# Optimization experiments

Hardware: AMD Instinct MI355X
Metric: run time of the kernel (lower is better)

The kernel has to match this reference:

```python
import jax, jax.numpy as jnp
import numpy as np

B, C, L = 128, 12, 1024
N_DIL, DIV, H, K, KSZ, NCP = 7, 2, 32, 8, 9, 6


def setup_inputs() -> dict:
    key = jax.random.key(0)
    kx, kw, ki = jax.random.split(key, 3)
    X = jax.random.normal(kx, (B, C, L), dtype=jnp.float32)
    W = jax.random.normal(kw, (N_DIL, DIV, K * H, 1, KSZ), dtype=jnp.float32)
    # Hydra weight normalization: zero mean, unit L1 norm along the kernel taps
    W = W - W.mean(-1, keepdims=True)
    W = W / jnp.abs(W).sum(-1, keepdims=True)
    I = jax.random.randint(ki, (N_DIL, DIV, H, NCP), 0, C, dtype=jnp.int32)
    return {"X": X, "W": W, "I": I}


def _forward(X, W, I):
    b = X.shape[0]
    diff_X = X[..., 1:] - X[..., :-1]  # first-order difference series
    bi = jnp.arange(b)[:, None, None]
    hi = jnp.arange(H)[None, :, None]
    Z = []
    for di in range(N_DIL):
        d = 2 ** di
        p = (KSZ - 1) * d // 2  # 'same' padding -> output length == input length
        for j in range(DIV):
            src = X if j == 0 else diff_X
            # irregular channel gather + sum over selected channels: [b, H, L']
            g = src[:, I[di, j]].sum(2)
            # grouped dilated conv1d: groups=H, k=K outputs per group -> [b, K*H, L']
            y = jax.lax.conv_general_dilated(
                g, W[di, j], window_strides=(1,), padding=[(p, p)],
                rhs_dilation=(d,), dimension_numbers=("NCH", "OIH", "NCH"),
                feature_group_count=H)
            y = y.reshape(b, H, K, -1)  # [b, H, K, L'] (group-major channel order)
            mx = y.max(2)               # [b, H, L']
            amx = y.argmax(2)
            amn = y.argmin(2)
            # scatter_add histograms over which kernel won at each position
            count_max = jnp.zeros((b, H, K), y.dtype).at[bi, hi, amx].add(mx)
            count_min = jnp.zeros((b, H, K), y.dtype).at[bi, hi, amn].add(jnp.ones_like(mx))
            Z.append(count_max)
            Z.append(count_min)
    return jnp.concatenate(Z, axis=1).reshape(b, -1)


def reference(X, W, I):
    return _forward(X, W, I)
```

## Files before the change

### kernel.cpp

```cpp
#include <hip/hip_runtime.h>

#define NB 128
#define NC 12
#define NL 1024
#define NDIL 7
#define NDIV 2
#define NH 32
#define NK 8
#define NKSZ 9
#define NNCP 6
#define OUTPB (NDIL*NDIV*2*NH*NK)

#define SER_STRIDE 1280
#define LDS_FLOATS (4*SER_STRIDE + 256)

__device__ __forceinline__ float4 ld4(const float* p) { return *(const float4*)p; }

__device__ __forceinline__ float sgpr(float v) {
    return __int_as_float(__builtin_amdgcn_readfirstlane(__float_as_int(v)));
}

template<int CTRL, int RM>
__device__ __forceinline__ float dppadd_f(float x) {
    int t = __builtin_amdgcn_update_dpp(0, __float_as_int(x), CTRL, RM, 0xf, false);
    return x + __int_as_float(t);
}
template<int CTRL, int RM>
__device__ __forceinline__ unsigned dppadd_u(unsigned x) {
    int t = __builtin_amdgcn_update_dpp(0, (int)x, CTRL, RM, 0xf, false);
    return x + (unsigned)t;
}
#define RSUM_F(x) { x = dppadd_f<0x111,0xf>(x); x = dppadd_f<0x112,0xf>(x); \
                    x = dppadd_f<0x114,0xf>(x); x = dppadd_f<0x118,0xf>(x); \
                    x = dppadd_f<0x142,0xa>(x); x = dppadd_f<0x143,0xc>(x); }
#define RSUM_U(x) { x = dppadd_u<0x111,0xf>(x); x = dppadd_u<0x112,0xf>(x); \
                    x = dppadd_u<0x114,0xf>(x); x = dppadd_u<0x118,0xf>(x); \
                    x = dppadd_u<0x142,0xa>(x); x = dppadd_u<0x143,0xc>(x); }

#define Wk(k,t) wf[(k)*NKSZ+(t)]

__global__ __launch_bounds__(256) void hydra_kernel(
    const float* __restrict__ X,
    const float* __restrict__ W,
    const int*   __restrict__ I,
    float*       __restrict__ out)
{
    __shared__ float lds[LDS_FLOATS];
    __shared__ float red[4][16];

    const int bid = blockIdx.x;
    const int h4 = bid & 7;
    const int dj = (bid >> 3) % 14;
    const int b  = (bid >> 3) / 14;
    const int di = dj >> 1;
    const int j  = dj & 1;
    const int d  = 1 << di;

    const int tid  = threadIdx.x;
    const int lane = tid & 63;
    const int wid  = __builtin_amdgcn_readfirstlane(tid >> 6);
    const int h    = h4 * 4 + wid;
    const int Sw   = 256 + wid * SER_STRIDE;

    #pragma unroll
    for (int z = 0; z < 5; ++z) lds[z * SER_STRIDE + tid] = 0.f;

    const int* idx = I + ((di*NDIV + j)*NH + h)*NNCP;
    const float* xb = X + (size_t)b * NC * NL;
    const float* p0 = xb + idx[0]*NL;
    const float* p1 = xb + idx[1]*NL;
    const float* p2 = xb + idx[2]*NL;
    const float* p3 = xb + idx[3]*NL;
    const float* p4 = xb + idx[4]*NL;
    const float* p5 = xb + idx[5]*NL;

    if (j == 0) {
        #pragma unroll
        for (int c = 0; c < 4; ++c) {
            const int e = 256*c + 4*lane;
            float4 v0 = ld4(p0+e), v1 = ld4(p1+e), v2 = ld4(p2+e);
            float4 v3 = ld4(p3+e), v4 = ld4(p4+e), v5 = ld4(p5+e);
            float4 s;
            s.x = v0.x+v1.x+v2.x+v3.x+v4.x+v5.x;
            s.y = v0.y+v1.y+v2.y+v3.y+v4.y+v5.y;
            s.z = v0.z+v1.z+v2.z+v3.z+v4.z+v5.z;
            s.w = v0.w+v1.w+v2.w+v3.w+v4.w+v5.w;
            *(float4*)(lds + Sw + e) = s;
        }
    } else {
        float4 sa[4];
        #pragma unroll
        for (int c = 0; c < 4; ++c) {
            const int e = 256*c + 4*lane;
            float4 v0 = ld4(p0+e), v1 = ld4(p1+e), v2 = ld4(p2+e);
            float4 v3 = ld4(p3+e), v4 = ld4(p4+e), v5 = ld4(p5+e);
            sa[c].x = v0.x+v1.x+v2.x+v3.x+v4.x+v5.x;
            sa[c].y = v0.y+v1.y+v2.y+v3.y+v4.y+v5.y;
            sa[c].z = v0.z+v1.z+v2.z+v3.z+v4.z+v5.z;
            sa[c].w = v0.w+v1.w+v2.w+v3.w+v4.w+v5.w;
        }
        #pragma unroll
        for (int c = 0; c < 4; ++c) {
            const float nxt = (c < 3) ? __shfl(sa[(c+1) & 3].x, 0, 64) : 0.f;
            const float sh  = __shfl_down(sa[c].x, 1, 64);
            const float Se4 = (lane == 63) ? nxt : sh;
            float4 df;
            df.x = sa[c].y - sa[c].x;
            df.y = sa[c].z - sa[c].y;
            df.z = sa[c].w - sa[c].z;
            df.w = Se4 - sa[c].w;
            if (c == 3 && lane == 63) df.w = 0.f;
            const int e = 256*c + 4*lane;
            *(float4*)(lds + Sw + e) = df;
        }
    }
    __syncthreads();

    float wf[NK*NKSZ];
    {
        const float* Wp = W + (size_t)((di*NDIV + j)*(NK*NH) + h*NK) * NKSZ;
        #pragma unroll
        for (int i = 0; i < 18; ++i) {
            float4 v = ld4(Wp + 4*i);
            wf[4*i+0] = sgpr(v.x); wf[4*i+1] = sgpr(v.y);
            wf[4*i+2] = sgpr(v.z); wf[4*i+3] = sgpr(v.w);
        }
    }

    float    cm[NK];
    unsigned cn[NK];
    #pragma unroll
    for (int k = 0; k < NK; ++k) { cm[k] = 0.f; cn[k] = 0u; }

    const int  base = Sw + 2*lane;
    const bool okl  = (j == 0) || (lane != 63);

#define ARGBIN(A, OK)                                                     \
    {                                                                     \
        float mx = fmaxf(fmaxf(A[0], A[1]), A[2]);                        \
        mx = fmaxf(fmaxf(mx, A[3]), A[4]);                                \
        mx = fmaxf(fmaxf(mx, A[5]), A[6]);                                \
        mx = fmaxf(mx, A[7]);                                             \
        float mn = fminf(fminf(A[0], A[1]), A[2]);                        \
        mn = fminf(fminf(mn, A[3]), A[4]);                                \
        mn = fminf(fminf(mn, A[5]), A[6]);                                \
        mn = fminf(mn, A[7]);                                             \
        if (OK) {                                                         \
            _Pragma("unroll")                                             \
            for (int k = 0; k < NK; ++k) {                                \
                cm[k] += (A[k] == mx) ? A[k] : 0.f;                       \
                cn[k] += (A[k] == mn) ? 1u : 0u;                          \
            }                                                             \
        }                                                                 \
    }

    if (d == 1) {
        for (int c = 0; c < 8; ++c) {
            const float* bp = lds + base - 4 + 128*c;
            float2 q0 = *(const float2*)(bp);
            float2 q1 = *(const float2*)(bp + 2);
            float2 q2 = *(const float2*)(bp + 4);
            float2 q3 = *(const float2*)(bp + 6);
            float2 q4 = *(const float2*)(bp + 8);
            const float win[10] = { q0.x,q0.y,q1.x,q1.y,q2.x,q2.y,q3.x,q3.y,q4.x,q4.y };
            float a0[NK], a1[NK];
            #pragma unroll
            for (int k = 0; k < NK; ++k) { a0[k] = 0.f; a1[k] = 0.f; }
            #pragma unroll
            for (int t = 0; t < NKSZ; ++t)
                #pragma unroll
                for (int k = 0; k < NK; ++k) {
                    a0[k] = fmaf(Wk(k,t), win[t],   a0[k]);
                    a1[k] = fmaf(Wk(k,t), win[t+1], a1[k]);
                }
            ARGBIN(a0, true);
            ARGBIN(a1, (c != 7) || okl);
        }
    } else {
        for (int c = 0; c < 8; ++c) {
            float2 v[NKSZ];
            #pragma unroll
            for (int t = 0; t < NKSZ; ++t)
                v[t] = *(const float2*)(lds + base + (t - 4)*d + 128*c);
            float a0[NK], a1[NK];
            #pragma unroll
            for (int k = 0; k < NK; ++k) { a0[k] = 0.f; a1[k] = 0.f; }
            #pragma unroll
            for (int t = 0; t < NKSZ; ++t)
                #pragma unroll
                for (int k = 0; k < NK; ++k) {
                    a0[k] = fmaf(Wk(k,t), v[t].x, a0[k]);
                    a1[k] = fmaf(Wk(k,t), v[t].y, a1[k]);
                }
            ARGBIN(a0, true);
            ARGBIN(a1, (c != 7) || okl);
        }
    }
#undef ARGBIN

    unsigned cp[4];
    #pragma unroll
    for (int i = 0; i < 4; ++i) cp[i] = cn[2*i] | (cn[2*i+1] << 16);

    #pragma unroll
    for (int k = 0; k < NK; ++k) RSUM_F(cm[k]);
    #pragma unroll
    for (int i = 0; i < 4; ++i) RSUM_U(cp[i]);

    if (lane == 63) {
        #pragma unroll
        for (int k = 0; k < NK; ++k) red[wid][k] = cm[k];
        #pragma unroll
        for (int i = 0; i < 4; ++i) {
            red[wid][8 + 2*i] = (float)(cp[i] & 0xffffu);
            red[wid][9 + 2*i] = (float)(cp[i] >> 16);
        }
    }
    __syncthreads();

    if (tid < 64) {
        const int ws = tid >> 4, slot = tid & 15;
        const int mm = slot >> 3, k = slot & 7;
        const int ho = h4*4 + ws;
        const int z  = dj*2 + mm;
        out[(size_t)b*OUTPB + z*(NH*NK) + ho*NK + k] = red[ws][slot];
    }
}

extern "C" void kernel_launch(void* const* d_in, const int* in_sizes, int n_in,
                              void* d_out, int out_size, void* d_ws, size_t ws_size,
                              hipStream_t stream) {
    const float* X = (const float*)d_in[0];
    const float* W = (const float*)d_in[1];
    const int*   I = (const int*)d_in[2];
    float* out = (float*)d_out;

    const int nblocks = NB * (NDIL*NDIV) * (NH/4);
    hydra_kernel<<<dim3(nblocks), dim3(256), 0, stream>>>(X, W, I, out);
}
```

Measured before the change: 164.1 us.

## Use packed fp16 dot2 for dilated conv taps and drop block barriers

Measured after the change: 189.1 us. +15.2%, slower.

```diff
diff --git a/kernel.cpp b/kernel.cpp
--- a/kernel.cpp
+++ b/kernel.cpp
@@ -14,10 +14,22 @@
 #define SER_STRIDE 1280
 #define LDS_FLOATS (4*SER_STRIDE + 256)
 
+typedef __fp16 h2 __attribute__((ext_vector_type(2)));
+
 __device__ __forceinline__ float4 ld4(const float* p) { return *(const float4*)p; }
 
-__device__ __forceinline__ float sgpr(float v) {
+__device__ __forceinline__ float sgpr_f(float v) {
     return __int_as_float(__builtin_amdgcn_readfirstlane(__float_as_int(v)));
+}
+__device__ __forceinline__ h2 sgpr_h2(h2 v) {
+    int i = __builtin_amdgcn_readfirstlane(__builtin_bit_cast(int, v));
+    return __builtin_bit_cast(h2, i);
+}
+__device__ __forceinline__ h2 pkrtz(float x, float y) {
+    return __builtin_amdgcn_cvt_pkrtz(x, y);
+}
+__device__ __forceinline__ float dot2(h2 a, h2 b, float c) {
+    return __builtin_amdgcn_fdot2(a, b, c, false);
 }
 
 template<int CTRL, int RM>
@@ -36,8 +48,6 @@
 #define RSUM_U(x) { x = dppadd_u<0x111,0xf>(x); x = dppadd_u<0x112,0xf>(x); \
                     x = dppadd_u<0x114,0xf>(x); x = dppadd_u<0x118,0xf>(x); \
                     x = dppadd_u<0x142,0xa>(x); x = dppadd_u<0x143,0xc>(x); }
-
-#define Wk(k,t) wf[(k)*NKSZ+(t)]
 
 __global__ __launch_bounds__(256) void hydra_kernel(
     const float* __restrict__ X,
@@ -46,7 +56,6 @@
     float*       __restrict__ out)
 {
     __shared__ float lds[LDS_FLOATS];
-    __shared__ float red[4][16];
 
     const int bid = blockIdx.x;
     const int h4 = bid & 7;
@@ -63,7 +72,10 @@
     const int Sw   = 256 + wid * SER_STRIDE;
 
     #pragma unroll
-    for (int z = 0; z < 5; ++z) lds[z * SER_STRIDE + tid] = 0.f;
+    for (int z = 0; z < 2; ++z) {
+        float4 zz; zz.x = 0.f; zz.y = 0.f; zz.z = 0.f; zz.w = 0.f;
+        *(float4*)(lds + (wid + z) * SER_STRIDE + 4 * lane) = zz;
+    }
 
     const int* idx = I + ((di*NDIV + j)*NH + h)*NNCP;
     const float* xb = X + (size_t)b * NC * NL;
@@ -114,16 +126,17 @@
             *(float4*)(lds + Sw + e) = df;
         }
     }
-    __syncthreads();
-
-    float wf[NK*NKSZ];
+
+    h2    wp[NK][4];
+    float w8[NK];
     {
         const float* Wp = W + (size_t)((di*NDIV + j)*(NK*NH) + h*NK) * NKSZ;
         #pragma unroll
-        for (int i = 0; i < 18; ++i) {
-            float4 v = ld4(Wp + 4*i);
-            wf[4*i+0] = sgpr(v.x); wf[4*i+1] = sgpr(v.y);
-            wf[4*i+2] = sgpr(v.z); wf[4*i+3] = sgpr(v.w);
+        for (int k = 0; k < NK; ++k) {
+            #pragma unroll
+            for (int t = 0; t < 4; ++t)
+                wp[k][t] = sgpr_h2(pkrtz(Wp[k*NKSZ + 2*t], Wp[k*NKSZ + 2*t + 1]));
+            w8[k] = sgpr_f(Wp[k*NKSZ + 8]);
         }
     }
 
@@ -163,35 +176,52 @@
             float2 q3 = *(const float2*)(bp + 6);
             float2 q4 = *(const float2*)(bp + 8);
             const float win[10] = { q0.x,q0.y,q1.x,q1.y,q2.x,q2.y,q3.x,q3.y,q4.x,q4.y };
+            h2 pk[8];
+            #pragma unroll
+            for (int i = 0; i < 8; ++i) pk[i] = pkrtz(win[i], win[i+1]);
             float a0[NK], a1[NK];
             #pragma unroll
-            for (int k = 0; k < NK; ++k) { a0[k] = 0.f; a1[k] = 0.f; }
-            #pragma unroll
-            for (int t = 0; t < NKSZ; ++t)
-                #pragma unroll
-                for (int k = 0; k < NK; ++k) {
-                    a0[k] = fmaf(Wk(k,t), win[t],   a0[k]);
-                    a1[k] = fmaf(Wk(k,t), win[t+1], a1[k]);
-                }
+            for (int k = 0; k < NK; ++k) {
+                a0[k] = dot2(wp[k][0], pk[0], 0.f);
+                a0[k] = dot2(wp[k][1], pk[2], a0[k]);
+                a0[k] = dot2(wp[k][2], pk[4], a0[k]);
+                a0[k] = dot2(wp[k][3], pk[6], a0[k]);
+                a0[k] = fmaf(w8[k], win[8], a0[k]);
+                a1[k] = dot2(wp[k][0], pk[1], 0.f);
+                a1[k] = dot2(wp[k][1], pk[3], a1[k]);
+                a1[k] = dot2(wp[k][2], pk[5], a1[k]);
+                a1[k] = dot2(wp[k][3], pk[7], a1[k]);
+                a1[k] = fmaf(w8[k], win[9], a1[k]);
+            }
             ARGBIN(a0, true);
             ARGBIN(a1, (c != 7) || okl);
         }
     } else {
         for (int c = 0; c < 8; ++c) {
-            float2 v[NKSZ];
+            float2 r[NKSZ];
             #pragma unroll
             for (int t = 0; t < NKSZ; ++t)
-                v[t] = *(const float2*)(lds + base + (t - 4)*d + 128*c);
+                r[t] = *(const float2*)(lds + base + (t - 4)*d + 128*c);
+            h2 pa[4], pb[4];
+            #pragma unroll
+            for (int tp = 0; tp < 4; ++tp) {
+                pa[tp] = pkrtz(r[2*tp].x, r[2*tp+1].x);
+                pb[tp] = pkrtz(r[2*tp].y, r[2*tp+1].y);
+            }
             float a0[NK], a1[NK];
             #pragma unroll
-            for (int k = 0; k < NK; ++k) { a0[k] = 0.f; a1[k] = 0.f; }
-            #pragma unroll
-            for (int t = 0; t < NKSZ; ++t)
-                #pragma unroll
-                for (int k = 0; k < NK; ++k) {
-                    a0[k] = fmaf(Wk(k,t), v[t].x, a0[k]);
-                    a1[k] = fmaf(Wk(k,t), v[t].y, a1[k]);
-                }
+            for (int k = 0; k < NK; ++k) {
+                a0[k] = dot2(wp[k][0], pa[0], 0.f);
+                a0[k] = dot2(wp[k][1], pa[1], a0[k]);
+                a0[k] = dot2(wp[k][2], pa[2], a0[k]);
+                a0[k] = dot2(wp[k][3], pa[3], a0[k]);
+                a0[k] = fmaf(w8[k], r[8].x, a0[k]);
+                a1[k] = dot2(wp[k][0], pb[0], 0.f);
+                a1[k] = dot2(wp[k][1], pb[1], a1[k]);
+                a1[k] = dot2(wp[k][2], pb[2], a1[k]);
+                a1[k] = dot2(wp[k][3], pb[3], a1[k]);
+                a1[k] = fmaf(w8[k], r[8].y, a1[k]);
+            }
             ARGBIN(a0, true);
             ARGBIN(a1, (c != 7) || okl);
         }
@@ -208,22 +238,15 @@
     for (int i = 0; i < 4; ++i) RSUM_U(cp[i]);
 
     if (lane == 63) {
-        #pragma unroll
-        for (int k = 0; k < NK; ++k) red[wid][k] = cm[k];
+        float* ob = out + (size_t)b*OUTPB + (dj*2)*(NH*NK) + h*NK;
+        #pragma unroll
+        for (int k = 0; k < NK; ++k) ob[k] = cm[k];
+        float* oc = ob + NH*NK;
         #pragma unroll
         for (int i = 0; i < 4; ++i) {
-            red[wid][8 + 2*i] = (float)(cp[i] & 0xffffu);
-            red[wid][9 + 2*i] = (float)(cp[i] >> 16);
-        }
-    }
-    __syncthreads();
-
-    if (tid < 64) {
-        const int ws = tid >> 4, slot = tid & 15;
-        const int mm = slot >> 3, k = slot & 7;
-        const int ho = h4*4 + ws;
-        const int z  = dj*2 + mm;
-        out[(size_t)b*OUTPB + z*(NH*NK) + ho*NK + k] = red[ws][slot];
+            oc[2*i]     = (float)(cp[i] & 0xffffu);
+            oc[2*i + 1] = (float)(cp[i] >> 16);
+        }
     }
 }
 
```

## Specialize conv per dilation and drop block barriers with wave-private LDS

Applied to the files above, without the earlier changes.

Measured after the change: 159.1 us. -3.0%, faster.

```diff
diff --git a/kernel.cpp b/kernel.cpp
--- a/kernel.cpp
+++ b/kernel.cpp
@@ -16,7 +16,7 @@
 
 __device__ __forceinline__ float4 ld4(const float* p) { return *(const float4*)p; }
 
-__device__ __forceinline__ float sgpr(float v) {
+__device__ __forceinline__ float sgpr_f(float v) {
     return __int_as_float(__builtin_amdgcn_readfirstlane(__float_as_int(v)));
 }
 
@@ -38,102 +38,6 @@
                     x = dppadd_u<0x142,0xa>(x); x = dppadd_u<0x143,0xc>(x); }
 
 #define Wk(k,t) wf[(k)*NKSZ+(t)]
-
-__global__ __launch_bounds__(256) void hydra_kernel(
-    const float* __restrict__ X,
-    const float* __restrict__ W,
-    const int*   __restrict__ I,
-    float*       __restrict__ out)
-{
-    __shared__ float lds[LDS_FLOATS];
-    __shared__ float red[4][16];
-
-    const int bid = blockIdx.x;
-    const int h4 = bid & 7;
-    const int dj = (bid >> 3) % 14;
-    const int b  = (bid >> 3) / 14;
-    const int di = dj >> 1;
-    const int j  = dj & 1;
-    const int d  = 1 << di;
-
-    const int tid  = threadIdx.x;
-    const int lane = tid & 63;
-    const int wid  = __builtin_amdgcn_readfirstlane(tid >> 6);
-    const int h    = h4 * 4 + wid;
-    const int Sw   = 256 + wid * SER_STRIDE;
-
-    #pragma unroll
-    for (int z = 0; z < 5; ++z) lds[z * SER_STRIDE + tid] = 0.f;
-
-    const int* idx = I + ((di*NDIV + j)*NH + h)*NNCP;
-    const float* xb = X + (size_t)b * NC * NL;
-    const float* p0 = xb + idx[0]*NL;
-    const float* p1 = xb + idx[1]*NL;
-    const float* p2 = xb + idx[2]*NL;
-    const float* p3 = xb + idx[3]*NL;
-    const float* p4 = xb + idx[4]*NL;
-    const float* p5 = xb + idx[5]*NL;
-
-    if (j == 0) {
-        #pragma unroll
-        for (int c = 0; c < 4; ++c) {
-            const int e = 256*c + 4*lane;
-            float4 v0 = ld4(p0+e), v1 = ld4(p1+e), v2 = ld4(p2+e);
-            float4 v3 = ld4(p3+e), v4 = ld4(p4+e), v5 = ld4(p5+e);
-            float4 s;
-            s.x = v0.x+v1.x+v2.x+v3.x+v4.x+v5.x;
-            s.y = v0.y+v1.y+v2.y+v3.y+v4.y+v5.y;
-            s.z = v0.z+v1.z+v2.z+v3.z+v4.z+v5.z;
-            s.w = v0.w+v1.w+v2.w+v3.w+v4.w+v5.w;
-            *(float4*)(lds + Sw + e) = s;
-        }
-    } else {
-        float4 sa[4];
-        #pragma unroll
-        for (int c = 0; c < 4; ++c) {
-            const int e = 256*c + 4*lane;
-            float4 v0 = ld4(p0+e), v1 = ld4(p1+e), v2 = ld4(p2+e);
-            float4 v3 = ld4(p3+e), v4 = ld4(p4+e), v5 = ld4(p5+e);
-            sa[c].x = v0.x+v1.x+v2.x+v3.x+v4.x+v5.x;
-            sa[c].y = v0.y+v1.y+v2.y+v3.y+v4.y+v5.y;
-            sa[c].z = v0.z+v1.z+v2.z+v3.z+v4.z+v5.z;
-            sa[c].w = v0.w+v1.w+v2.w+v3.w+v4.w+v5.w;
-        }
-        #pragma unroll
-        for (int c = 0; c < 4; ++c) {
-            const float nxt = (c < 3) ? __shfl(sa[(c+1) & 3].x, 0, 64) : 0.f;
-            const float sh  = __shfl_down(sa[c].x, 1, 64);
-            const float Se4 = (lane == 63) ? nxt : sh;
-            float4 df;
-            df.x = sa[c].y - sa[c].x;
-            df.y = sa[c].z - sa[c].y;
-            df.z = sa[c].w - sa[c].z;
-            df.w = Se4 - sa[c].w;
-            if (c == 3 && lane == 63) df.w = 0.f;
-            const int e = 256*c + 4*lane;
-            *(float4*)(lds + Sw + e) = df;
-        }
-    }
-    __syncthreads();
-
-    float wf[NK*NKSZ];
-    {
-        const float* Wp = W + (size_t)((di*NDIV + j)*(NK*NH) + h*NK) * NKSZ;
-        #pragma unroll
-        for (int i = 0; i < 18; ++i) {
-            float4 v = ld4(Wp + 4*i);
-            wf[4*i+0] = sgpr(v.x); wf[4*i+1] = sgpr(v.y);
-            wf[4*i+2] = sgpr(v.z); wf[4*i+3] = sgpr(v.w);
-        }
-    }
-
-    float    cm[NK];
-    unsigned cn[NK];
-    #pragma unroll
-    for (int k = 0; k < NK; ++k) { cm[k] = 0.f; cn[k] = 0u; }
-
-    const int  base = Sw + 2*lane;
-    const bool okl  = (j == 0) || (lane != 63);
 
 #define ARGBIN(A, OK)                                                     \
     {                                                                     \
@@ -154,9 +58,13 @@
         }                                                                 \
     }
 
-    if (d == 1) {
-        for (int c = 0; c < 8; ++c) {
-            const float* bp = lds + base - 4 + 128*c;
+template<int D>
+__device__ __forceinline__ void conv_body(const float* __restrict__ bp0,
+                                          const float (&wf)[NK*NKSZ], bool okl,
+                                          float (&cm)[NK], unsigned (&cn)[NK]) {
+    if constexpr (D == 1) {
+        const float* bp = bp0 - 4;
+        for (int c = 0; c < 8; ++c, bp += 128) {
             float2 q0 = *(const float2*)(bp);
             float2 q1 = *(const float2*)(bp + 2);
             float2 q2 = *(const float2*)(bp + 4);
@@ -177,11 +85,12 @@
             ARGBIN(a1, (c != 7) || okl);
         }
     } else {
-        for (int c = 0; c < 8; ++c) {
-            float2 v[NKSZ];
+        const float* bp = bp0 - 4*D;
+        for (int c = 0; c < 8; ++c, bp += 128) {
+            float2 r[NKSZ];
             #pragma unroll
             for (int t = 0; t < NKSZ; ++t)
-                v[t] = *(const float2*)(lds + base + (t - 4)*d + 128*c);
+                r[t] = *(const float2*)(bp + t*D);
             float a0[NK], a1[NK];
             #pragma unroll
             for (int k = 0; k < NK; ++k) { a0[k] = 0.f; a1[k] = 0.f; }
@@ -189,14 +98,120 @@
             for (int t = 0; t < NKSZ; ++t)
                 #pragma unroll
                 for (int k = 0; k < NK; ++k) {
-                    a0[k] = fmaf(Wk(k,t), v[t].x, a0[k]);
-                    a1[k] = fmaf(Wk(k,t), v[t].y, a1[k]);
+                    a0[k] = fmaf(Wk(k,t), r[t].x, a0[k]);
+                    a1[k] = fmaf(Wk(k,t), r[t].y, a1[k]);
                 }
             ARGBIN(a0, true);
             ARGBIN(a1, (c != 7) || okl);
         }
     }
-#undef ARGBIN
+}
+
+__global__ __launch_bounds__(256) void hydra_kernel(
+    const float* __restrict__ X,
+    const float* __restrict__ W,
+    const int*   __restrict__ I,
+    float*       __restrict__ out)
+{
+    __shared__ float lds[LDS_FLOATS];
+
+    const int bid = blockIdx.x;
+    const int h4 = bid & 7;
+    const int dj = (bid >> 3) % 14;
+    const int b  = (bid >> 3) / 14;
+    const int di = dj >> 1;
+    const int j  = dj & 1;
+
+    const int tid  = threadIdx.x;
+    const int lane = tid & 63;
+    const int wid  = __builtin_amdgcn_readfirstlane(tid >> 6);
+    const int h    = h4 * 4 + wid;
+    const int Sw   = 256 + wid * SER_STRIDE;
+
+    #pragma unroll
+    for (int z = 0; z < 2; ++z) {
+        float4 zz; zz.x = 0.f; zz.y = 0.f; zz.z = 0.f; zz.w = 0.f;
+        *(float4*)(lds + (wid + z) * SER_STRIDE + 4 * lane) = zz;
+    }
+
+    const int* idx = I + ((di*NDIV + j)*NH + h)*NNCP;
+    const float* xb = X + (size_t)b * NC * NL;
+    const float* p0 = xb + idx[0]*NL;
+    const float* p1 = xb + idx[1]*NL;
+    const float* p2 = xb + idx[2]*NL;
+    const float* p3 = xb + idx[3]*NL;
+    const float* p4 = xb + idx[4]*NL;
+    const float* p5 = xb + idx[5]*NL;
+
+    if (j == 0) {
+        #pragma unroll
+        for (int c = 0; c < 4; ++c) {
+            const int e = 256*c + 4*lane;
+            float4 v0 = ld4(p0+e), v1 = ld4(p1+e), v2 = ld4(p2+e);
+            float4 v3 = ld4(p3+e), v4 = ld4(p4+e), v5 = ld4(p5+e);
+            float4 s;
+            s.x = v0.x+v1.x+v2.x+v3.x+v4.x+v5.x;
+            s.y = v0.y+v1.y+v2.y+v3.y+v4.y+v5.y;
+            s.z = v0.z+v1.z+v2.z+v3.z+v4.z+v5.z;
+            s.w = v0.w+v1.w+v2.w+v3.w+v4.w+v5.w;
+            *(float4*)(lds + Sw + e) = s;
+        }
+    } else {
+        float4 sa[4];
+        #pragma unroll
+        for (int c = 0; c < 4; ++c) {
+            const int e = 256*c + 4*lane;
+            float4 v0 = ld4(p0+e), v1 = ld4(p1+e), v2 = ld4(p2+e);
+            float4 v3 = ld4(p3+e), v4 = ld4(p4+e), v5 = ld4(p5+e);
+            sa[c].x = v0.x+v1.x+v2.x+v3.x+v4.x+v5.x;
+            sa[c].y = v0.y+v1.y+v2.y+v3.y+v4.y+v5.y;
+            sa[c].z = v0.z+v1.z+v2.z+v3.z+v4.z+v5.z;
+            sa[c].w = v0.w+v1.w+v2.w+v3.w+v4.w+v5.w;
+        }
+        #pragma unroll
+        for (int c = 0; c < 4; ++c) {
+            const float nxt = (c < 3) ? __shfl(sa[(c+1) & 3].x, 0, 64) : 0.f;
+            const float sh  = __shfl_down(sa[c].x, 1, 64);
+            const float Se4 = (lane == 63) ? nxt : sh;
+            float4 df;
+            df.x = sa[c].y - sa[c].x;
+            df.y = sa[c].z - sa[c].y;
+            df.z = sa[c].w - sa[c].z;
+            df.w = Se4 - sa[c].w;
+            if (c == 3 && lane == 63) df.w = 0.f;
+            const int e = 256*c + 4*lane;
+            *(float4*)(lds + Sw + e) = df;
+        }
+    }
+
+    float wf[NK*NKSZ];
+    {
+        const float* Wp = W + (size_t)((di*NDIV + j)*(NK*NH) + h*NK) * NKSZ;
+        #pragma unroll
+        for (int i = 0; i < 18; ++i) {
+            float4 v = ld4(Wp + 4*i);
+            wf[4*i+0] = sgpr_f(v.x); wf[4*i+1] = sgpr_f(v.y);
+            wf[4*i+2] = sgpr_f(v.z); wf[4*i+3] = sgpr_f(v.w);
+        }
+    }
+
+    float    cm[NK];
+    unsigned cn[NK];
+    #pragma unroll
+    for (int k = 0; k < NK; ++k) { cm[k] = 0.f; cn[k] = 0u; }
+
+    const float* bp0 = lds + Sw + 2*lane;
+    const bool   okl = (j == 0) || (lane != 63);
+
+    switch (di) {
+        case 0: conv_body<1>( bp0, wf, okl, cm, cn); break;
+        case 1: conv_body<2>( bp0, wf, okl, cm, cn); break;
+        case 2: conv_body<4>( bp0, wf, okl, cm, cn); break;
+        case 3: conv_body<8>( bp0, wf, okl, cm, cn); break;
+        case 4: conv_body<16>(bp0, wf, okl, cm, cn); break;
+        case 5: conv_body<32>(bp0, wf, okl, cm, cn); break;
+        default: conv_body<64>(bp0, wf, okl, cm, cn); break;
+    }
 
     unsigned cp[4];
     #pragma unroll
@@ -208,22 +223,15 @@
     for (int i = 0; i < 4; ++i) RSUM_U(cp[i]);
 
     if (lane == 63) {
-        #pragma unroll
-        for (int k = 0; k < NK; ++k) red[wid][k] = cm[k];
+        float* ob = out + (size_t)b*OUTPB + (dj*2)*(NH*NK) + h*NK;
+        #pragma unroll
+        for (int k = 0; k < NK; ++k) ob[k] = cm[k];
+        float* oc = ob + NH*NK;
         #pragma unroll
         for (int i = 0; i < 4; ++i) {
-            red[wid][8 + 2*i] = (float)(cp[i] & 0xffffu);
-            red[wid][9 + 2*i] = (float)(cp[i] >> 16);
-        }
-    }
-    __syncthreads();
-
-    if (tid < 64) {
-        const int ws = tid >> 4, slot = tid & 15;
-        const int mm = slot >> 3, k = slot & 7;
-        const int ho = h4*4 + ws;
-        const int z  = dj*2 + mm;
-        out[(size_t)b*OUTPB + z*(NH*NK) + ho*NK + k] = red[ws][slot];
+            oc[2*i]     = (float)(cp[i] & 0xffffu);
+            oc[2*i + 1] = (float)(cp[i] >> 16);
+        }
     }
 }
 
```
